# Performance work log

Hardware: AMD Instinct MI355X
Metric: run time of the kernel (lower is better)

## Reference

```python
import jax, jax.numpy as jnp
import numpy as np

DT = 0.02
Z_DIM = 32
U_DIM = 16


def _mlp(x, layers):
    # layers: list of (W, b); SiLU between all but last layer
    n = len(layers)
    for i, (W, b) in enumerate(layers):
        x = x @ W + b
        if i < n - 1:
            x = jax.nn.silu(x)
    return x


def _forward(x, u,
             e_w1, e_b1, e_w2, e_b2, e_w3, e_b3,
             d_w1, d_b1, d_w2, d_b2, d_w3, d_b3, d_w4, d_b4,
             a_w1, a_b1, a_w2, a_b2, a_w3, a_b3,
             b_w1, b_b1, b_w2, b_b2, b_w3, b_b3):
    # encode
    z = _mlp(x, [(e_w1, e_b1), (e_w2, e_b2), (e_w3, e_b3)])          # (B, Z)
    # state-dependent A(x) parameters: pairs (a_i, b_i) per 2x2 block
    aux = _mlp(x, [(a_w1, a_b1), (a_w2, a_b2), (a_w3, a_b3)])        # (B, Z)
    a = aux[:, 0::2]                                                  # (B, Z/2)
    b = aux[:, 1::2]
    f = jnp.exp(a * DT)
    c = jnp.cos(b * DT)
    s = jnp.sin(b * DT)
    # A(x) @ z without materializing block-diagonal: per-pair rotation-scale
    z0 = z[:, 0::2]
    z1 = z[:, 1::2]
    Az = jnp.stack([f * (c * z0 - s * z1), f * (s * z0 + c * z1)], axis=-1).reshape(z.shape)
    # B(x) @ u
    Bmat = _mlp(x, [(b_w1, b_b1), (b_w2, b_b2), (b_w3, b_b3)]).reshape(-1, Z_DIM, U_DIM)
    Bu = jnp.einsum('bzu,bu->bz', Bmat, u)
    # latent Euler step + decode
    z_next = z + DT * (Az + Bu)
    return _mlp(z_next, [(d_w1, d_b1), (d_w2, d_b2), (d_w3, d_b3), (d_w4, d_b4)])


def setup_inputs() -> dict:
    key = jax.random.key(0)
    ks = iter(jax.random.split(key, 32))
    def w(shape, scale=0.02):
        return jax.random.normal(next(ks), shape, jnp.float32) * scale
    B, X, U, Z, H, A = 16384, 64, 16, 32, 1024, 256
    return {
        'x': jax.random.normal(next(ks), (B, X), jnp.float32),
        'u': jax.random.normal(next(ks), (B, U), jnp.float32),
        'e_w1': w((X, H)), 'e_b1': w((H,)),
        'e_w2': w((H, H)), 'e_b2': w((H,)),
        'e_w3': w((H, Z)), 'e_b3': w((Z,)),
        'd_w1': w((Z, H)), 'd_b1': w((H,)),
        'd_w2': w((H, H)), 'd_b2': w((H,)),
        'd_w3': w((H, H)), 'd_b3': w((H,)),
        'd_w4': w((H, X)), 'd_b4': w((X,)),
        'a_w1': w((X, A)), 'a_b1': w((A,)),
        'a_w2': w((A, A)), 'a_b2': w((A,)),
        'a_w3': w((A, Z)), 'a_b3': w((Z,)),
        'b_w1': w((X, A)), 'b_b1': w((A,)),
        'b_w2': w((A, A)), 'b_b2': w((A,)),
        'b_w3': w((A, Z * U)), 'b_b3': w((Z * U,)),
    }


def reference(x, u,
              e_w1, e_b1, e_w2, e_b2, e_w3, e_b3,
              d_w1, d_b1, d_w2, d_b2, d_w3, d_b3, d_w4, d_b4,
              a_w1, a_b1, a_w2, a_b2, a_w3, a_b3,
              b_w1, b_b1, b_w2, b_b2, b_w3, b_b3):
    return _forward(x, u,
                    e_w1, e_b1, e_w2, e_b2, e_w3, e_b3,
                    d_w1, d_b1, d_w2, d_b2, d_w3, d_b3, d_w4, d_b4,
                    a_w1, a_b1, a_w2, a_b2, a_w3, a_b3,
                    b_w1, b_b1, b_w2, b_b2, b_w3, b_b3)
```

## Files before the change

### kernel.cpp

```cpp
#include <hip/hip_runtime.h>
#include <cstdint>
#include <cstddef>

#define B_SZ 16384
#define X_D  64
#define U_D  16
#define Z_D  32
#define H_D  1024
#define A_D  256
#define DT_C 0.02f

typedef _Float16 f16;
typedef f16   f16x8 __attribute__((ext_vector_type(8)));
typedef f16   f16x4 __attribute__((ext_vector_type(4)));
typedef float f32x4 __attribute__((ext_vector_type(4)));
typedef float f32x16 __attribute__((ext_vector_type(16)));

#define AS1 __attribute__((address_space(1)))
#define AS3 __attribute__((address_space(3)))

__device__ __forceinline__ void gld_lds16(const void* g, void* l) {
    __builtin_amdgcn_global_load_lds((AS1 void*)(g), (AS3 void*)(l), 16, 0, 0);
}

#define BARX()  do { asm volatile("" ::: "memory"); __builtin_amdgcn_s_barrier(); \
                     asm volatile("" ::: "memory"); } while (0)
#define LGK0()  do { asm volatile("s_waitcnt lgkmcnt(0)" ::: "memory"); \
                     __builtin_amdgcn_sched_barrier(0); } while (0)
#define WAITV0() asm volatile("s_waitcnt vmcnt(0)" ::: "memory")

struct GArg {
    const f16*  A;
    const f16*  W;
    const float* bias;
    void*       C;
    int lda, ldc, K;
};
struct GSet { GArg g[3]; int yn0, yn1; };

template<int BM,int BN,int BK,int WM,int WN,bool SILU,int OM>
__launch_bounds__(256)
__global__ void gemm_k(GSet p)
{
    static_assert(OM != 1 || BN == 128, "OM1 repack assumes BN=128");
    int yb = blockIdx.y, gi = 0;
    if (yb >= p.yn0) { yb -= p.yn0; gi = 1; if (yb >= p.yn1) { yb -= p.yn1; gi = 2; } }
    const GArg ga = p.g[gi];

    constexpr int SEGROW = BK / 8;
    constexpr int SMASK  = (SEGROW < 8 ? SEGROW : 8) - 1;
    constexpr int WTM = BM / WM, WTN = BN / WN;
    static_assert(WTM % 32 == 0 && WTN % 32 == 0, "wave tile in 32x32 units");
    constexpr int RM = WTM / 32, RN = WTN / 32;
    constexpr int KS = BK / 16;
    constexpr int ITA = (BM * SEGROW) / 256;
    constexpr int ITB = (BN * SEGROW) / 256;

    constexpr int STAGE_B = (BM + BN) * BK * 2;
    constexpr int CS_B    = (OM == 1) ? BM * BN * 2 : 0;
    constexpr int SMEM_B  = STAGE_B > CS_B ? STAGE_B : CS_B;
    __shared__ __align__(16) char smem[SMEM_B];
    f16* As = (f16*)smem;
    f16* Bs = As + BM * BK;

    const int tid  = threadIdx.x;
    const int lane = tid & 63;
    const int wave = tid >> 6;
    const int wm = wave / WN, wn = wave % WN;
    const int l31 = lane & 31, half = lane >> 5;

    const size_t arow0 = (size_t)blockIdx.x * BM;
    const size_t brow0 = (size_t)yb * BN;
    const int lda = ga.lda, K = ga.K;

    const f16* aptr[ITA];
    const f16* bptr[ITB];
#pragma unroll
    for (int it = 0; it < ITA; ++it) {
        int s = it * 256 + tid;
        int row = s / SEGROW, st = s % SEGROW;
        int sg = st ^ (row & SMASK);
        aptr[it] = ga.A + (arow0 + row) * lda + sg * 8;
    }
#pragma unroll
    for (int it = 0; it < ITB; ++it) {
        int s = it * 256 + tid;
        int row = s / SEGROW, st = s % SEGROW;
        int sg = st ^ (row & SMASK);
        bptr[it] = ga.W + (brow0 + row) * K + sg * 8;
    }

    f32x16 acc[RM][RN];
#pragma unroll
    for (int i = 0; i < RM; ++i)
#pragma unroll
        for (int j = 0; j < RN; ++j)
#pragma unroll
            for (int r = 0; r < 16; ++r) acc[i][j][r] = 0.f;

    for (int k0 = 0; k0 < K; k0 += BK) {
#pragma unroll
        for (int it = 0; it < ITA; ++it) {
            gld_lds16(aptr[it], &As[(it * 256 + tid) * 8]);
            aptr[it] += BK;
        }
#pragma unroll
        for (int it = 0; it < ITB; ++it) {
            gld_lds16(bptr[it], &Bs[(it * 256 + tid) * 8]);
            bptr[it] += BK;
        }
        __syncthreads();

#pragma unroll
        for (int ks = 0; ks < KS; ++ks) {
            f16x8 af[RM], bf[RN];
#pragma unroll
            for (int i = 0; i < RM; ++i) {
                int row = wm * WTM + i * 32 + l31;
                int st  = (ks * 2 + half) ^ (row & SMASK);
                af[i] = *(const f16x8*)&As[(row * SEGROW + st) * 8];
            }
#pragma unroll
            for (int j = 0; j < RN; ++j) {
                int row = wn * WTN + j * 32 + l31;
                int st  = (ks * 2 + half) ^ (row & SMASK);
                bf[j] = *(const f16x8*)&Bs[(row * SEGROW + st) * 8];
            }
#pragma unroll
            for (int i = 0; i < RM; ++i)
#pragma unroll
                for (int j = 0; j < RN; ++j)
                    acc[i][j] = __builtin_amdgcn_mfma_f32_32x32x16_f16(
                        af[i], bf[j], acc[i][j], 0, 0, 0);
        }
        __syncthreads();
    }

    const int rowbL = wm * WTM;
    const int colbL = wn * WTN;

    if constexpr (OM == 1) {
        f16* Cs = (f16*)smem;
#pragma unroll
        for (int j = 0; j < RN; ++j) {
            int colL = colbL + j * 32 + l31;
            float bv = ga.bias[(int)brow0 + colL];
            int chL = colL >> 3, wi = colL & 7;
#pragma unroll
            for (int i = 0; i < RM; ++i) {
#pragma unroll
                for (int r = 0; r < 16; ++r) {
                    int rowL = rowbL + i * 32 + (r & 3) + 8 * (r >> 2) + 4 * half;
                    float v = acc[i][j][r] + bv;
                    if (SILU) v = v / (1.0f + __expf(-v));
                    Cs[rowL * BN + ((chL ^ (rowL & 15)) << 3) + wi] = (f16)v;
                }
            }
        }
        __syncthreads();
        f16* Cout = (f16*)ga.C;
#pragma unroll
        for (int pass = 0; pass < (BM * BN / 8) / 256; ++pass) {
            int s = pass * 256 + tid;
            int rowL = s >> 4;
            int ch = s & 15;
            f16x8 v = *(const f16x8*)&Cs[rowL * BN + ((ch ^ (rowL & 15)) << 3)];
            *(f16x8*)&Cout[(size_t)(arow0 + rowL) * ga.ldc + brow0 + ch * 8] = v;
        }
    } else {
        float* Cout = (float*)ga.C;
#pragma unroll
        for (int j = 0; j < RN; ++j) {
            int col = (int)brow0 + colbL + j * 32 + l31;
            float bv = ga.bias[col];
#pragma unroll
            for (int i = 0; i < RM; ++i) {
#pragma unroll
                for (int r = 0; r < 16; ++r) {
                    int row = (int)arow0 + rowbL + i * 32
                            + (r & 3) + 8 * (r >> 2) + 4 * half;
                    float v = acc[i][j][r] + bv;
                    if (SILU) v = v / (1.0f + __expf(-v));
                    Cout[(size_t)row * ga.ldc + col] = v;
                }
            }
        }
    }
}

template<bool SILU>
__launch_bounds__(512, 2)
__global__ void gemm10_k(GSet p)
{
    int yb = blockIdx.y, gi = 0;
    if (yb >= p.yn0) { yb -= p.yn0; gi = 1; if (yb >= p.yn1) { yb -= p.yn1; gi = 2; } }
    const GArg ga = p.g[gi];

    __shared__ __align__(16) char smem[131072];

    const int tid  = threadIdx.x;
    const int lane = tid & 63, wave = tid >> 6;
    const int wm = wave >> 2, wn = wave & 3;
    const int l15 = lane & 15, quad = lane >> 4;

    const size_t arow0 = (size_t)blockIdx.x * 256;
    const size_t brow0 = (size_t)yb * 256;
    const int lda = ga.lda, K = ga.K;
    const int nt = K >> 6;

    const f16* spA[4];
    const f16* spB[4];
#pragma unroll
    for (int q = 0; q < 4; ++q) {
        int s = q * 512 + tid;
        int row = s >> 3;
        int kseg = (s & 7) ^ (row & 7);
        spA[q] = ga.A + (arow0 + row) * lda + kseg * 8;
        spB[q] = ga.W + (brow0 + row) * K + kseg * 8;
    }

    f32x4 acc[8][4];
#pragma unroll
    for (int i = 0; i < 8; ++i)
#pragma unroll
        for (int j = 0; j < 4; ++j)
#pragma unroll
            for (int r = 0; r < 4; ++r) acc[i][j][r] = 0.f;

    auto stageA = [&](char* buf, int q) {
        gld_lds16(spA[q], buf + (size_t)(q * 512 + tid) * 16);
        spA[q] += 64;
    };
    auto stageB = [&](char* buf, int q) {
        gld_lds16(spB[q], buf + 32768 + (size_t)(q * 512 + tid) * 16);
        spB[q] += 64;
    };

    f16x8 af[4][2], bf[2][2];
    auto readA = [&](const char* buf, int mh) {
#pragma unroll
        for (int i = 0; i < 4; ++i) {
            int ar = wm * 128 + mh * 64 + i * 16 + l15;
#pragma unroll
            for (int ks = 0; ks < 2; ++ks) {
                int st = (ks * 4 + quad) ^ (ar & 7);
                af[i][ks] = *(const f16x8*)(buf + ar * 128 + st * 16);
            }
        }
    };
    auto readB = [&](const char* buf, int nh) {
#pragma unroll
        for (int j = 0; j < 2; ++j) {
            int br = wn * 64 + nh * 32 + j * 16 + l15;
#pragma unroll
            for (int ks = 0; ks < 2; ++ks) {
                int st = (ks * 4 + quad) ^ (br & 7);
                bf[j][ks] = *(const f16x8*)(buf + 32768 + br * 128 + st * 16);
            }
        }
    };
    auto mma = [&](int mh, int nh) {
        __builtin_amdgcn_s_setprio(1);
#pragma unroll
        for (int ks = 0; ks < 2; ++ks)
#pragma unroll
            for (int i = 0; i < 4; ++i)
#pragma unroll
                for (int j = 0; j < 2; ++j)
                    acc[mh * 4 + i][nh * 2 + j] =
                        __builtin_amdgcn_mfma_f32_16x16x32_f16(
                            af[i][ks], bf[j][ks], acc[mh * 4 + i][nh * 2 + j],
                            0, 0, 0);
        __builtin_amdgcn_s_setprio(0);
    };

    {
        char* b0 = smem;
        stageB(b0, 0); stageB(b0, 1); stageB(b0, 2); stageB(b0, 3);
        stageA(b0, 0); stageA(b0, 1); stageA(b0, 2); stageA(b0, 3);
        WAITV0();
        BARX();
    }

    for (int t = 0; t < nt; ++t) {
        char* buf  = smem + (size_t)(t & 1) * 65536;
        char* nbuf = smem + (size_t)((t & 1) ^ 1) * 65536;
        const bool st = (t + 1 < nt);
        readA(buf, 0); readB(buf, 0);
        if (st) { stageB(nbuf, 0); stageB(nbuf, 1); stageB(nbuf, 2); stageB(nbuf, 3); }
        BARX(); LGK0(); mma(0, 0); BARX();
        readB(buf, 1);
        if (st) { stageA(nbuf, 0); stageA(nbuf, 1); stageA(nbuf, 2); stageA(nbuf, 3); }
        BARX(); LGK0(); mma(0, 1); BARX();
        readA(buf, 1);
        BARX(); LGK0(); mma(1, 1); BARX();
        readB(buf, 0);
        if (st) WAITV0();
        BARX(); LGK0(); mma(1, 0); BARX();
    }

    f16* Cs = (f16*)smem;
#pragma unroll
    for (int mf = 0; mf < 8; ++mf)
#pragma unroll
        for (int nf = 0; nf < 4; ++nf) {
            int colL = wn * 64 + (nf >> 1) * 32 + (nf & 1) * 16 + l15;
            float bv = ga.bias[(int)brow0 + colL];
            int ch = colL >> 3, wi = colL & 7;
#pragma unroll
            for (int r = 0; r < 4; ++r) {
                int rowL = wm * 128 + (mf >> 2) * 64 + (mf & 3) * 16 + quad * 4 + r;
                float v = acc[mf][nf][r] + bv;
                if (SILU) v = v / (1.0f + __expf(-v));
                Cs[rowL * 256 + ((ch ^ (rowL & 31)) << 3) + wi] = (f16)v;
            }
        }
    __syncthreads();
    f16* Cout = (f16*)ga.C;
#pragma unroll
    for (int pass = 0; pass < 16; ++pass) {
        int s = pass * 512 + tid;
        int rowL = s >> 5, ch = s & 31;
        f16x8 v = *(const f16x8*)&Cs[rowL * 256 + ((ch ^ (rowL & 31)) << 3)];
        *(f16x8*)&Cout[(size_t)(arow0 + rowL) * ga.ldc + brow0 + ch * 8] = v;
    }
}

__launch_bounds__(256)
__global__ void mid_k(const f16* __restrict__ cc2,
                      const f16* __restrict__ e_w3t, const float* __restrict__ e_b3,
                      const f16* __restrict__ a_w3t, const float* __restrict__ a_b3,
                      const f16* __restrict__ b_w3t, const float* __restrict__ b_b3,
                      const float* __restrict__ u,   f16* __restrict__ znb)
{
    __shared__ __align__(16) f16 As[32 * 64];
    __shared__ __align__(16) f16 Bs[128 * 64];
    __shared__ float zb[32 * 32];
    __shared__ float ab[32 * 32];
    __shared__ float bu[32 * 32];
    __shared__ float ub[32 * 16];

    const int tid  = threadIdx.x;
    const int lane = tid & 63, wave = tid >> 6;
    const int l15 = lane & 15, quad = lane >> 4;
    const int r0 = blockIdx.x * 32;

    ub[tid]       = u[r0 * 16 + tid];
    ub[tid + 256] = u[r0 * 16 + 256 + tid];

#pragma unroll 1
    for (int ph = 0; ph < 2; ++ph) {
        const f16* W    = ph ? a_w3t : e_w3t;
        const float* bs = ph ? a_b3 : e_b3;
        const int K     = ph ? 256 : 1024;
        const int co    = ph ? 1024 : 0;
        float* ob       = ph ? ab : zb;
        f32x4 acc = {0.f, 0.f, 0.f, 0.f};
        for (int k0 = 0; k0 < K; k0 += 64) {
            {
                int row = tid >> 3, sg = (tid & 7) ^ (row & 7);
                gld_lds16(cc2 + (size_t)(r0 + row) * 1536 + co + k0 + sg * 8,
                          &As[tid * 8]);
            }
            {
                int row = tid >> 3, sg = (tid & 7) ^ (row & 7);
                gld_lds16(W + (size_t)row * K + k0 + sg * 8, &Bs[tid * 8]);
            }
            __syncthreads();
#pragma unroll
            for (int kk = 0; kk < 64; kk += 32) {
                int ar = ((wave >> 1) << 4) + l15;
                int ast = ((kk >> 3) + quad) ^ (ar & 7);
                f16x8 af = *(const f16x8*)&As[(ar * 8 + ast) * 8];
                int br = ((wave & 1) << 4) + l15;
                int bst = ((kk >> 3) + quad) ^ (br & 7);
                f16x8 bf = *(const f16x8*)&Bs[(br * 8 + bst) * 8];
                acc = __builtin_amdgcn_mfma_f32_16x16x32_f16(af, bf, acc, 0, 0, 0);
            }
            __syncthreads();
        }
#pragma unroll
        for (int r = 0; r < 4; ++r) {
            int row = ((wave >> 1) << 4) + quad * 4 + r;
            int col = ((wave & 1) << 4) + l15;
            ob[row * 32 + col] = acc[r] + bs[col];
        }
    }

#pragma unroll 1
    for (int ch = 0; ch < 4; ++ch) {
        f32x4 acc[2][2];
#pragma unroll
        for (int i = 0; i < 2; ++i)
#pragma unroll
            for (int j = 0; j < 2; ++j) acc[i][j] = f32x4{0.f, 0.f, 0.f, 0.f};
        for (int k0 = 0; k0 < 256; k0 += 64) {
            {   int row = tid >> 3, sg = (tid & 7) ^ (row & 7);
                gld_lds16(cc2 + (size_t)(r0 + row) * 1536 + 1280 + k0 + sg * 8,
                          &As[tid * 8]);
            }
#pragma unroll
            for (int it = 0; it < 4; ++it) {
                int s = it * 256 + tid;
                int row = s >> 3, sg = (s & 7) ^ (row & 7);
                gld_lds16(b_w3t + (size_t)(ch * 128 + row) * 256 + k0 + sg * 8,
                          &Bs[s * 8]);
            }
            __syncthreads();
#pragma unroll
            for (int kk = 0; kk < 64; kk += 32) {
                f16x8 af[2], bf[2];
#pragma unroll
                for (int i = 0; i < 2; ++i) {
                    int ar = i * 16 + l15;
                    int st = ((kk >> 3) + quad) ^ (ar & 7);
                    af[i] = *(const f16x8*)&As[(ar * 8 + st) * 8];
                }
#pragma unroll
                for (int j = 0; j < 2; ++j) {
                    int br = wave * 32 + j * 16 + l15;
                    int st = ((kk >> 3) + quad) ^ (br & 7);
                    bf[j] = *(const f16x8*)&Bs[(br * 8 + st) * 8];
                }
#pragma unroll
                for (int i = 0; i < 2; ++i)
#pragma unroll
                    for (int j = 0; j < 2; ++j)
                        acc[i][j] = __builtin_amdgcn_mfma_f32_16x16x32_f16(
                            af[i], bf[j], acc[i][j], 0, 0, 0);
            }
            __syncthreads();
        }
#pragma unroll
        for (int j = 0; j < 2; ++j) {
            int colg = ch * 128 + wave * 32 + j * 16 + l15;
            float bv = b_b3[colg];
            int z = colg >> 4;
#pragma unroll
            for (int i = 0; i < 2; ++i) {
#pragma unroll
                for (int r = 0; r < 4; ++r) {
                    int row = i * 16 + quad * 4 + r;
                    float v = (acc[i][j][r] + bv) * ub[row * 16 + l15];
                    v += __shfl_xor(v, 8, 16);
                    v += __shfl_xor(v, 4, 16);
                    v += __shfl_xor(v, 2, 16);
                    v += __shfl_xor(v, 1, 16);
                    if (l15 == 0) bu[row * 32 + z] = v;
                }
            }
        }
    }
    __syncthreads();

#pragma unroll
    for (int t = 0; t < 4; ++t) {
        int idx = t * 256 + tid;
        int row = idx >> 5, z = idx & 31;
        int pb = idx & ~1;
        float a  = ab[pb], b = ab[pb + 1];
        float z0 = zb[pb], z1 = zb[pb + 1];
        float f  = __expf(a * DT_C);
        float c_ = __cosf(b * DT_C);
        float s_ = __sinf(b * DT_C);
        float Az = (z & 1) ? f * (s_ * z0 + c_ * z1) : f * (c_ * z0 - s_ * z1);
        float zc = (z & 1) ? z1 : z0;
        znb[(size_t)(r0 + row) * 32 + z] = (f16)(zc + DT_C * (Az + bu[idx]));
    }
}

struct PrepArgs {
    const float* w[13];
    f16*         wt[13];
    int          K[13];
    int          N[13];
    const float* bsrc[3];
    float*       bias1;
    const float* x;
    f16*         xb;
};

__launch_bounds__(256)
__global__ void prep_k(PrepArgs pa, int ntrans, int ncvt)
{
    int bid = blockIdx.x;
    if (bid < ntrans) {
        int i = 0, t;
        for (;; ++i) {
            t = (pa.K[i] >> 5) * (pa.N[i] >> 5);
            if (bid < t) break;
            bid -= t;
        }
        const int K = pa.K[i], N = pa.N[i];
        const int tn = N >> 5;
        const int k0 = (bid / tn) << 5, n0 = (bid % tn) << 5;
        __shared__ float tbuf[32][33];
        const int tx = threadIdx.x & 31, ty = threadIdx.x >> 5;
        const float* src = pa.w[i];
        f16* dst = pa.wt[i];
#pragma unroll
        for (int r = 0; r < 32; r += 8)
            tbuf[ty + r][tx] = src[(size_t)(k0 + ty + r) * N + n0 + tx];
        __syncthreads();
#pragma unroll
        for (int r = 0; r < 32; r += 8)
            dst[(size_t)(n0 + ty + r) * K + k0 + tx] = (f16)tbuf[tx][ty + r];
    } else if (bid < ntrans + ncvt) {
        int i = ((bid - ntrans) * 256 + threadIdx.x) * 4;
        float4 v = *(const float4*)(pa.x + i);
        f16x4 o = {(f16)v.x, (f16)v.y, (f16)v.z, (f16)v.w};
        *(f16x4*)(pa.xb + i) = o;
    } else {
        int idx = (bid - ntrans - ncvt) * 256 + (int)threadIdx.x;
        float v = (idx < 1024) ? pa.bsrc[0][idx]
                : (idx < 1280) ? pa.bsrc[1][idx - 1024]
                               : pa.bsrc[2][idx - 1280];
        pa.bias1[idx] = v;
    }
}

extern "C" void kernel_launch(void* const* d_in, const int* in_sizes, int n_in,
                              void* d_out, int out_size, void* d_ws, size_t ws_size,
                              hipStream_t stream)
{
    (void)in_sizes; (void)n_in; (void)out_size; (void)ws_size;
    const float* x    = (const float*)d_in[0];
    const float* u    = (const float*)d_in[1];
    const float* e_w1 = (const float*)d_in[2];  const float* e_b1 = (const float*)d_in[3];
    const float* e_w2 = (const float*)d_in[4];  const float* e_b2 = (const float*)d_in[5];
    const float* e_w3 = (const float*)d_in[6];  const float* e_b3 = (const float*)d_in[7];
    const float* d_w1 = (const float*)d_in[8];  const float* d_b1 = (const float*)d_in[9];
    const float* d_w2 = (const float*)d_in[10]; const float* d_b2 = (const float*)d_in[11];
    const float* d_w3 = (const float*)d_in[12]; const float* d_b3 = (const float*)d_in[13];
    const float* d_w4 = (const float*)d_in[14]; const float* d_b4 = (const float*)d_in[15];
    const float* a_w1 = (const float*)d_in[16]; const float* a_b1 = (const float*)d_in[17];
    const float* a_w2 = (const float*)d_in[18]; const float* a_b2 = (const float*)d_in[19];
    const float* a_w3 = (const float*)d_in[20]; const float* a_b3 = (const float*)d_in[21];
    const float* b_w1 = (const float*)d_in[22]; const float* b_b1 = (const float*)d_in[23];
    const float* b_w2 = (const float*)d_in[24]; const float* b_b2 = (const float*)d_in[25];
    const float* b_w3 = (const float*)d_in[26]; const float* b_b3 = (const float*)d_in[27];

    char* p = (char*)d_ws;
    auto alloc = [&](size_t nbytes) -> void* {
        void* r = (void*)p;
        p += (nbytes + 255) & ~(size_t)255;
        return r;
    };
    f16*   xb   = (f16*)  alloc((size_t)B_SZ * X_D * 2);
    f16*   cc1  = (f16*)  alloc((size_t)B_SZ * 1536 * 2);
    f16*   cc2  = (f16*)  alloc((size_t)B_SZ * 1536 * 2);
    f16*   znb  = (f16*)  alloc((size_t)B_SZ * Z_D * 2);
    f16*   h1d  = cc1;
    f16*   h2d  = cc2;
    f16*   h3d  = cc1;
    f16*   W1t   = (f16*)alloc((size_t)1536 * X_D * 2);
    float* bias1 = (float*)alloc(1536 * 4);
    f16* e_w2t = (f16*)alloc((size_t)H_D * H_D * 2);
    f16* e_w3t = (f16*)alloc((size_t)Z_D * H_D * 2);
    f16* d_w1t = (f16*)alloc((size_t)H_D * Z_D * 2);
    f16* d_w2t = (f16*)alloc((size_t)H_D * H_D * 2);
    f16* d_w3t = (f16*)alloc((size_t)H_D * H_D * 2);
    f16* d_w4t = (f16*)alloc((size_t)X_D * H_D * 2);
    f16* a_w2t = (f16*)alloc((size_t)A_D * A_D * 2);
    f16* a_w3t = (f16*)alloc((size_t)Z_D * A_D * 2);
    f16* b_w2t = (f16*)alloc((size_t)A_D * A_D * 2);
    f16* b_w3t = (f16*)alloc((size_t)(Z_D * U_D) * A_D * 2);

    PrepArgs pa;
    const float* ws_[13] = {e_w1, e_w2, e_w3, d_w1, d_w2, d_w3, d_w4,
                            a_w1, a_w2, a_w3, b_w1, b_w2, b_w3};
    f16* wts_[13] = {W1t, e_w2t, e_w3t, d_w1t, d_w2t, d_w3t, d_w4t,
                     W1t + (size_t)1024 * X_D, a_w2t, a_w3t,
                     W1t + (size_t)1280 * X_D, b_w2t, b_w3t};
    int Ks_[13] = {X_D, H_D, H_D, Z_D, H_D, H_D, H_D, X_D, A_D, A_D, X_D, A_D, A_D};
    int Ns_[13] = {H_D, H_D, Z_D, H_D, H_D, H_D, X_D, A_D, A_D, Z_D, A_D, A_D, Z_D*U_D};
    int ntrans = 0;
    for (int i = 0; i < 13; ++i) {
        pa.w[i] = ws_[i]; pa.wt[i] = wts_[i]; pa.K[i] = Ks_[i]; pa.N[i] = Ns_[i];
        ntrans += (Ks_[i] >> 5) * (Ns_[i] >> 5);
    }
    pa.bsrc[0] = e_b1; pa.bsrc[1] = a_b1; pa.bsrc[2] = b_b1;
    pa.bias1 = bias1; pa.x = x; pa.xb = xb;
    const int ncvt = (B_SZ * X_D) / 1024;
    prep_k<<<ntrans + ncvt + 6, 256, 0, stream>>>(pa, ntrans, ncvt);

    auto G = [](const f16* A, const f16* W, const float* bias, void* C,
                int lda, int ldc, int K) {
        GArg g; g.A = A; g.W = W; g.bias = bias; g.C = C;
        g.lda = lda; g.ldc = ldc; g.K = K; return g;
    };
    GSet s;

    s.g[0] = G(xb, W1t, bias1, cc1, X_D, 1536, X_D);
    s.yn0 = 12; s.yn1 = 0;
    gemm_k<128,128,64,2,2,true,1><<<dim3(B_SZ/128, 12), 256, 0, stream>>>(s);

    s.g[0] = G(cc1,        e_w2t, e_b2, cc2,        1536, 1536, H_D);
    s.g[1] = G(cc1 + 1024, a_w2t, a_b2, cc2 + 1024, 1536, 1536, A_D);
    s.g[2] = G(cc1 + 1280, b_w2t, b_b2, cc2 + 1280, 1536, 1536, A_D);
    s.yn0 = 4; s.yn1 = 1;
    gemm10_k<true><<<dim3(B_SZ/256, 6), 512, 0, stream>>>(s);

    mid_k<<<B_SZ/32, 256, 0, stream>>>(cc2, e_w3t, e_b3, a_w3t, a_b3,
                                       b_w3t, b_b3, u, znb);

    s.yn0 = 8; s.yn1 = 0;
    s.g[0] = G(znb, d_w1t, d_b1, h1d, Z_D, H_D, Z_D);
    gemm_k<128,128,32,2,2,true,1><<<dim3(B_SZ/128, 8), 256, 0, stream>>>(s);

    s.yn0 = 4; s.yn1 = 0;
    s.g[0] = G(h1d, d_w2t, d_b2, h2d, H_D, H_D, H_D);
    gemm10_k<true><<<dim3(B_SZ/256, 4), 512, 0, stream>>>(s);

    s.g[0] = G(h2d, d_w3t, d_b3, h3d, H_D, H_D, H_D);
    gemm10_k<true><<<dim3(B_SZ/256, 4), 512, 0, stream>>>(s);

    s.g[0] = G(h3d, d_w4t, d_b4, d_out, H_D, X_D, H_D);
    s.yn0 = 1;
    gemm_k<64,64,64,2,2,false,0><<<dim3(B_SZ/64, 1), 256, 0, stream>>>(s);
}
```

Baseline: 349.0 us.

## Rework big GEMM to 4 waves with 128x128 per-wave tiles and simpler pipeline

The 256x256-tile GEMM now runs with 256 threads (4 waves) instead of 512. Each wave owns a 128x128 output sub-tile with 64 accumulators, so every fragment read from LDS feeds more MFMAs. The staged four-phase loop with explicit lgkmcnt waits and barriers is replaced by one prefetch of the next K tile, fragment reads for both k-halves, and a single barrier per iteration. The trade-off is far more registers per thread, with occupancy of one block per CU and possible spills, plus less interleaving of memory and MFMA work.

```diff
diff --git a/kernel.cpp b/kernel.cpp
--- a/kernel.cpp
+++ b/kernel.cpp
@@ -25,8 +25,6 @@
 
 #define BARX()  do { asm volatile("" ::: "memory"); __builtin_amdgcn_s_barrier(); \
                      asm volatile("" ::: "memory"); } while (0)
-#define LGK0()  do { asm volatile("s_waitcnt lgkmcnt(0)" ::: "memory"); \
-                     __builtin_amdgcn_sched_barrier(0); } while (0)
 #define WAITV0() asm volatile("s_waitcnt vmcnt(0)" ::: "memory")
 
 struct GArg {
@@ -189,8 +187,8 @@
 }
 
 template<bool SILU>
-__launch_bounds__(512, 2)
-__global__ void gemm10_k(GSet p)
+__launch_bounds__(256, 1)
+__global__ void gemm11_k(GSet p)
 {
     int yb = blockIdx.y, gi = 0;
     if (yb >= p.yn0) { yb -= p.yn0; gi = 1; if (yb >= p.yn1) { yb -= p.yn1; gi = 2; } }
@@ -200,7 +198,7 @@
 
     const int tid  = threadIdx.x;
     const int lane = tid & 63, wave = tid >> 6;
-    const int wm = wave >> 2, wn = wave & 3;
+    const int wm = wave >> 1, wn = wave & 1;
     const int l15 = lane & 15, quad = lane >> 4;
 
     const size_t arow0 = (size_t)blockIdx.x * 256;
@@ -208,118 +206,99 @@
     const int lda = ga.lda, K = ga.K;
     const int nt = K >> 6;
 
-    const f16* spA[4];
-    const f16* spB[4];
-#pragma unroll
-    for (int q = 0; q < 4; ++q) {
-        int s = q * 512 + tid;
-        int row = s >> 3;
-        int kseg = (s & 7) ^ (row & 7);
-        spA[q] = ga.A + (arow0 + row) * lda + kseg * 8;
-        spB[q] = ga.W + (brow0 + row) * K + kseg * 8;
-    }
-
-    f32x4 acc[8][4];
+    const f16* aptr;
+    const f16* bptr;
+    {
+        int row = tid >> 3;
+        int kseg = (tid & 7) ^ (row & 7);
+        aptr = ga.A + (arow0 + row) * lda + kseg * 8;
+        bptr = ga.W + (brow0 + row) * K + kseg * 8;
+    }
+    const size_t astep = (size_t)32 * lda;
+    const size_t bstep = (size_t)32 * K;
+
+    f32x4 acc[8][8];
 #pragma unroll
     for (int i = 0; i < 8; ++i)
 #pragma unroll
-        for (int j = 0; j < 4; ++j)
+        for (int j = 0; j < 8; ++j)
 #pragma unroll
             for (int r = 0; r < 4; ++r) acc[i][j][r] = 0.f;
 
-    auto stageA = [&](char* buf, int q) {
-        gld_lds16(spA[q], buf + (size_t)(q * 512 + tid) * 16);
-        spA[q] += 64;
+    auto stage = [&](char* buf) {
+#pragma unroll
+        for (int q = 0; q < 8; ++q)
+            gld_lds16(aptr + (size_t)q * astep, buf + q * 4096 + (size_t)tid * 16);
+#pragma unroll
+        for (int q = 0; q < 8; ++q)
+            gld_lds16(bptr + (size_t)q * bstep, buf + 32768 + q * 4096 + (size_t)tid * 16);
+        aptr += 64; bptr += 64;
     };
-    auto stageB = [&](char* buf, int q) {
-        gld_lds16(spB[q], buf + 32768 + (size_t)(q * 512 + tid) * 16);
-        spB[q] += 64;
+
+    f16x8 a0[8], b0[8], a1[8], b1[8];
+    auto readfr = [&](const char* buf, int ks, f16x8* a, f16x8* b) {
+#pragma unroll
+        for (int i = 0; i < 8; ++i) {
+            int ar = wm * 128 + i * 16 + l15;
+            int st = (ks * 4 + quad) ^ (ar & 7);
+            a[i] = *(const f16x8*)(buf + ar * 128 + st * 16);
+        }
+#pragma unroll
+        for (int j = 0; j < 8; ++j) {
+            int br = wn * 128 + j * 16 + l15;
+            int st = (ks * 4 + quad) ^ (br & 7);
+            b[j] = *(const f16x8*)(buf + 32768 + br * 128 + st * 16);
+        }
     };
-
-    f16x8 af[4][2], bf[2][2];
-    auto readA = [&](const char* buf, int mh) {
-#pragma unroll
-        for (int i = 0; i < 4; ++i) {
-            int ar = wm * 128 + mh * 64 + i * 16 + l15;
-#pragma unroll
-            for (int ks = 0; ks < 2; ++ks) {
-                int st = (ks * 4 + quad) ^ (ar & 7);
-                af[i][ks] = *(const f16x8*)(buf + ar * 128 + st * 16);
-            }
-        }
-    };
-    auto readB = [&](const char* buf, int nh) {
-#pragma unroll
-        for (int j = 0; j < 2; ++j) {
-            int br = wn * 64 + nh * 32 + j * 16 + l15;
-#pragma unroll
-            for (int ks = 0; ks < 2; ++ks) {
-                int st = (ks * 4 + quad) ^ (br & 7);
-                bf[j][ks] = *(const f16x8*)(buf + 32768 + br * 128 + st * 16);
-            }
-        }
-    };
-    auto mma = [&](int mh, int nh) {
+    auto mma = [&](const f16x8* a, const f16x8* b) {
         __builtin_amdgcn_s_setprio(1);
 #pragma unroll
-        for (int ks = 0; ks < 2; ++ks)
-#pragma unroll
-            for (int i = 0; i < 4; ++i)
-#pragma unroll
-                for (int j = 0; j < 2; ++j)
-                    acc[mh * 4 + i][nh * 2 + j] =
-                        __builtin_amdgcn_mfma_f32_16x16x32_f16(
-                            af[i][ks], bf[j][ks], acc[mh * 4 + i][nh * 2 + j],
-                            0, 0, 0);
+        for (int i = 0; i < 8; ++i)
+#pragma unroll
+            for (int j = 0; j < 8; ++j)
+                acc[i][j] = __builtin_amdgcn_mfma_f32_16x16x32_f16(
+                    a[i], b[j], acc[i][j], 0, 0, 0);
         __builtin_amdgcn_s_setprio(0);
     };
 
-    {
-        char* b0 = smem;
-        stageB(b0, 0); stageB(b0, 1); stageB(b0, 2); stageB(b0, 3);
-        stageA(b0, 0); stageA(b0, 1); stageA(b0, 2); stageA(b0, 3);
-        WAITV0();
-        BARX();
-    }
+    stage(smem);
+    WAITV0();
+    BARX();
 
     for (int t = 0; t < nt; ++t) {
         char* buf  = smem + (size_t)(t & 1) * 65536;
         char* nbuf = smem + (size_t)((t & 1) ^ 1) * 65536;
         const bool st = (t + 1 < nt);
-        readA(buf, 0); readB(buf, 0);
-        if (st) { stageB(nbuf, 0); stageB(nbuf, 1); stageB(nbuf, 2); stageB(nbuf, 3); }
-        BARX(); LGK0(); mma(0, 0); BARX();
-        readB(buf, 1);
-        if (st) { stageA(nbuf, 0); stageA(nbuf, 1); stageA(nbuf, 2); stageA(nbuf, 3); }
-        BARX(); LGK0(); mma(0, 1); BARX();
-        readA(buf, 1);
-        BARX(); LGK0(); mma(1, 1); BARX();
-        readB(buf, 0);
+        if (st) stage(nbuf);
+        readfr(buf, 0, a0, b0);
+        readfr(buf, 1, a1, b1);
+        mma(a0, b0);
+        mma(a1, b1);
         if (st) WAITV0();
-        BARX(); LGK0(); mma(1, 0); BARX();
+        BARX();
     }
 
     f16* Cs = (f16*)smem;
 #pragma unroll
-    for (int mf = 0; mf < 8; ++mf)
-#pragma unroll
-        for (int nf = 0; nf < 4; ++nf) {
-            int colL = wn * 64 + (nf >> 1) * 32 + (nf & 1) * 16 + l15;
-            float bv = ga.bias[(int)brow0 + colL];
-            int ch = colL >> 3, wi = colL & 7;
+    for (int j = 0; j < 8; ++j) {
+        int colL = wn * 128 + j * 16 + l15;
+        float bv = ga.bias[(int)brow0 + colL];
+        int ch = colL >> 3, wi = colL & 7;
+#pragma unroll
+        for (int i = 0; i < 8; ++i)
 #pragma unroll
             for (int r = 0; r < 4; ++r) {
-                int rowL = wm * 128 + (mf >> 2) * 64 + (mf & 3) * 16 + quad * 4 + r;
-                float v = acc[mf][nf][r] + bv;
+                int rowL = wm * 128 + i * 16 + quad * 4 + r;
+                float v = acc[i][j][r] + bv;
                 if (SILU) v = v / (1.0f + __expf(-v));
                 Cs[rowL * 256 + ((ch ^ (rowL & 31)) << 3) + wi] = (f16)v;
             }
-        }
+    }
     __syncthreads();
     f16* Cout = (f16*)ga.C;
 #pragma unroll
-    for (int pass = 0; pass < 16; ++pass) {
-        int s = pass * 512 + tid;
+    for (int pass = 0; pass < 32; ++pass) {
+        int s = pass * 256 + tid;
         int rowL = s >> 5, ch = s & 31;
         f16x8 v = *(const f16x8*)&Cs[rowL * 256 + ((ch ^ (rowL & 31)) << 3)];
         *(f16x8*)&Cout[(size_t)(arow0 + rowL) * ga.ldc + brow0 + ch * 8] = v;
@@ -599,7 +578,7 @@
     s.g[1] = G(cc1 + 1024, a_w2t, a_b2, cc2 + 1024, 1536, 1536, A_D);
     s.g[2] = G(cc1 + 1280, b_w2t, b_b2, cc2 + 1280, 1536, 1536, A_D);
     s.yn0 = 4; s.yn1 = 1;
-    gemm10_k<true><<<dim3(B_SZ/256, 6), 512, 0, stream>>>(s);
+    gemm11_k<true><<<dim3(B_SZ/256, 6), 256, 0, stream>>>(s);
 
     mid_k<<<B_SZ/32, 256, 0, stream>>>(cc2, e_w3t, e_b3, a_w3t, a_b3,
                                        b_w3t, b_b3, u, znb);
@@ -610,10 +589,10 @@
 
     s.yn0 = 4; s.yn1 = 0;
     s.g[0] = G(h1d, d_w2t, d_b2, h2d, H_D, H_D, H_D);
-    gemm10_k<true><<<dim3(B_SZ/256, 4), 512, 0, stream>>>(s);
+    gemm11_k<true><<<dim3(B_SZ/256, 4), 256, 0, stream>>>(s);
 
     s.g[0] = G(h2d, d_w3t, d_b3, h3d, H_D, H_D, H_D);
-    gemm10_k<true><<<dim3(B_SZ/256, 4), 512, 0, stream>>>(s);
+    gemm11_k<true><<<dim3(B_SZ/256, 4), 256, 0, stream>>>(s);
 
     s.g[0] = G(h3d, d_w4t, d_b4, d_out, H_D, X_D, H_D);
     s.yn0 = 1;
```

Result: slower. 374.7 us (+7.4%).

## Fuse decoder first layer GEMM into mid kernel epilogue

Applied to the files above, without the earlier changes.

The mid kernel now keeps the latent z_next tile in shared memory and computes the first decoder layer (K=32 to 1024) with SiLU directly, writing h1d. This removes the separate decoder-layer-1 GEMM launch and the znb round trip through global memory. It adds per-block staging of d_w1t in four 256-column chunks, with extra syncs. The h1d stores are scalar f16 writes per element, which may coalesce poorly and cost more than the old kernel's output path.

```diff
diff --git a/kernel.cpp b/kernel.cpp
--- a/kernel.cpp
+++ b/kernel.cpp
@@ -331,10 +331,12 @@
                       const f16* __restrict__ e_w3t, const float* __restrict__ e_b3,
                       const f16* __restrict__ a_w3t, const float* __restrict__ a_b3,
                       const f16* __restrict__ b_w3t, const float* __restrict__ b_b3,
-                      const float* __restrict__ u,   f16* __restrict__ znb)
+                      const f16* __restrict__ d_w1t, const float* __restrict__ d_b1,
+                      const float* __restrict__ u,   f16* __restrict__ h1d)
 {
     __shared__ __align__(16) f16 As[32 * 64];
     __shared__ __align__(16) f16 Bs[128 * 64];
+    __shared__ __align__(16) f16 zs[32 * 32];
     __shared__ float zb[32 * 32];
     __shared__ float ab[32 * 32];
     __shared__ float bu[32 * 32];
@@ -347,6 +349,17 @@
 
     ub[tid]       = u[r0 * 16 + tid];
     ub[tid + 256] = u[r0 * 16 + 256 + tid];
+
+    auto stage_d1 = [&](int ch) {
+#pragma unroll
+        for (int q = 0; q < 4; ++q) {
+            int s = q * 256 + tid;
+            int row = s >> 2, j = s & 3;
+            int kseg = j ^ (row & 3);
+            gld_lds16(d_w1t + (size_t)(ch * 256 + row) * 32 + kseg * 8,
+                      &Bs[s * 8]);
+        }
+    };
 
 #pragma unroll 1
     for (int ph = 0; ph < 2; ++ph) {
@@ -453,6 +466,7 @@
     }
     __syncthreads();
 
+    stage_d1(0);
 #pragma unroll
     for (int t = 0; t < 4; ++t) {
         int idx = t * 256 + tid;
@@ -465,7 +479,50 @@
         float s_ = __sinf(b * DT_C);
         float Az = (z & 1) ? f * (s_ * z0 + c_ * z1) : f * (c_ * z0 - s_ * z1);
         float zc = (z & 1) ? z1 : z0;
-        znb[(size_t)(r0 + row) * 32 + z] = (f16)(zc + DT_C * (Az + bu[idx]));
+        f16 zv = (f16)(zc + DT_C * (Az + bu[idx]));
+        zs[(row * 4 + ((z >> 3) ^ (row & 3))) * 8 + (z & 7)] = zv;
+    }
+    __syncthreads();
+
+    f16x8 afD[2];
+#pragma unroll
+    for (int i = 0; i < 2; ++i) {
+        int ar = i * 16 + l15;
+        int ast = quad ^ (ar & 3);
+        afD[i] = *(const f16x8*)&zs[(ar * 4 + ast) * 8];
+    }
+#pragma unroll 1
+    for (int ch = 0; ch < 4; ++ch) {
+        f32x4 accd[2][4];
+#pragma unroll
+        for (int n = 0; n < 4; ++n) {
+            int br = wave * 64 + n * 16 + l15;
+            int bst = quad ^ (br & 3);
+            f16x8 bf = *(const f16x8*)&Bs[(br * 4 + bst) * 8];
+#pragma unroll
+            for (int i = 0; i < 2; ++i) {
+                f32x4 zero = {0.f, 0.f, 0.f, 0.f};
+                accd[i][n] = __builtin_amdgcn_mfma_f32_16x16x32_f16(
+                    afD[i], bf, zero, 0, 0, 0);
+            }
+        }
+        __syncthreads();
+        if (ch < 3) stage_d1(ch + 1);
+#pragma unroll
+        for (int n = 0; n < 4; ++n) {
+            int col = ch * 256 + wave * 64 + n * 16 + l15;
+            float bv = d_b1[col];
+#pragma unroll
+            for (int i = 0; i < 2; ++i)
+#pragma unroll
+                for (int r = 0; r < 4; ++r) {
+                    int row = i * 16 + quad * 4 + r;
+                    float v = accd[i][n][r] + bv;
+                    v = v / (1.0f + __expf(-v));
+                    h1d[(size_t)(r0 + row) * 1024 + col] = (f16)v;
+                }
+        }
+        if (ch < 3) __syncthreads();
     }
 }
 
@@ -549,7 +606,6 @@
     f16*   xb   = (f16*)  alloc((size_t)B_SZ * X_D * 2);
     f16*   cc1  = (f16*)  alloc((size_t)B_SZ * 1536 * 2);
     f16*   cc2  = (f16*)  alloc((size_t)B_SZ * 1536 * 2);
-    f16*   znb  = (f16*)  alloc((size_t)B_SZ * Z_D * 2);
     f16*   h1d  = cc1;
     f16*   h2d  = cc2;
     f16*   h3d  = cc1;
@@ -602,11 +658,7 @@
     gemm10_k<true><<<dim3(B_SZ/256, 6), 512, 0, stream>>>(s);
 
     mid_k<<<B_SZ/32, 256, 0, stream>>>(cc2, e_w3t, e_b3, a_w3t, a_b3,
-                                       b_w3t, b_b3, u, znb);
-
-    s.yn0 = 8; s.yn1 = 0;
-    s.g[0] = G(znb, d_w1t, d_b1, h1d, Z_D, H_D, Z_D);
-    gemm_k<128,128,32,2,2,true,1><<<dim3(B_SZ/128, 8), 256, 0, stream>>>(s);
+                                       b_w3t, b_b3, d_w1t, d_b1, u, h1d);
 
     s.yn0 = 4; s.yn1 = 0;
     s.g[0] = G(h1d, d_w2t, d_b2, h2d, H_D, H_D, H_D);
```

Measured after the change: 347.8 us, median of 3. Within noise of the previous version (-0.4%).
